# Optimization experiments

Hardware: AMD Instinct MI355X
Metric: run time of the kernel (lower is better)

The kernel has to match this reference:

```python
import jax, jax.numpy as jnp
import numpy as np

HEADS = 6
HEAD_DIM = 64
OUT_DIM = HEADS * HEAD_DIM  # 384
NEG_SLOPE = 0.2
VERY_NEG = -1e9  # fp32 path in original


def setup_inputs() -> dict:
    key = jax.random.key(0)
    k1, k2, k3, k4, k5 = jax.random.split(key, 5)
    N, IN_DIM = 2048, 256
    h = jax.random.normal(k1, (N, IN_DIM), dtype=jnp.float32)
    adj = jax.random.randint(k2, (N, N), 0, 2).astype(jnp.float32)
    adj = jnp.maximum(adj, jnp.eye(N, dtype=jnp.float32))  # self-loops
    W_src = jax.random.normal(k3, (HEADS, IN_DIM, HEAD_DIM), dtype=jnp.float32) * 0.05
    W_dst = jax.random.normal(k4, (HEADS, IN_DIM, HEAD_DIM), dtype=jnp.float32) * 0.05
    a = jax.random.normal(k5, (HEADS, HEAD_DIM), dtype=jnp.float32) * 0.05
    bias = jnp.zeros((OUT_DIM,), dtype=jnp.float32)
    return {"h": h, "adj": adj, "W_src": W_src, "W_dst": W_dst, "a": a, "bias": bias}


def _gatv2(h, adj, W_src, W_dst, a, bias):
    N = h.shape[0]
    mask = adj > 0  # (N, N)
    Q = jnp.einsum('nd,hdf->hnf', h, W_src)  # (H, N, F)
    K = jnp.einsum('nd,hdf->hnf', h, W_dst)  # (H, N, F)
    outs, attns = [], []
    for i in range(HEADS):  # loop over small fixed head count to cap (N,N,F) intermediates
        s = Q[i][:, None, :] + K[i][None, :, :]          # (N, N, F)
        s = jnp.where(s >= 0, s, NEG_SLOPE * s)          # LeakyReLU
        e = jnp.einsum('ijf,f->ij', s, a[i])             # (N, N)
        e = jnp.where(mask, e, VERY_NEG)
        p = jax.nn.softmax(e, axis=-1)                   # stable (max-subtract) as in original
        outs.append(p @ K[i])                            # (N, F)
        attns.append(p)
    out = jnp.stack(outs, axis=0)                        # (H, N, F)
    h_prime = out.transpose(1, 0, 2).reshape(N, OUT_DIM) + bias  # concat heads
    attn_mean = jnp.mean(jnp.stack(attns, axis=0), axis=0)       # (N, N)
    return h_prime, attn_mean


def reference(h, adj, W_src, W_dst, a, bias):
    return _gatv2(h, adj, W_src, W_dst, a, bias)
```

## Files before the change

kernel.cpp:

```cpp
#include <hip/hip_runtime.h>

namespace {

constexpr int N_NODES = 2048;
constexpr int IN_DIM  = 256;
constexpr int HEADS   = 6;
constexpr int HD      = 64;
constexpr int OUT_DIM = HEADS * HD;

__global__ __launch_bounds__(64) void qk_proj(
    const float* __restrict__ hmat, const float* __restrict__ Wsrc,
    const float* __restrict__ Wdst, const float* __restrict__ a,
    float* __restrict__ Qw, float* __restrict__ Kw,
    float* __restrict__ qaw, float* __restrict__ kaw)
{
  const int f    = threadIdx.x;
  const int i    = blockIdx.x;
  const int head = blockIdx.y;
  const int z    = blockIdx.z;
  const float* __restrict__ W = (z ? Wdst : Wsrc) + (size_t)head * IN_DIM * HD;
  const float* __restrict__ hrow = hmat + (size_t)i * IN_DIM;

  float a0 = 0.f, a1 = 0.f, a2 = 0.f, a3 = 0.f;
  #pragma unroll 4
  for (int k = 0; k < IN_DIM; k += 4) {
    a0 = fmaf(hrow[k + 0], W[(k + 0) * HD + f], a0);
    a1 = fmaf(hrow[k + 1], W[(k + 1) * HD + f], a1);
    a2 = fmaf(hrow[k + 2], W[(k + 2) * HD + f], a2);
    a3 = fmaf(hrow[k + 3], W[(k + 3) * HD + f], a3);
  }
  const float acc = (a0 + a1) + (a2 + a3);
  (z ? Kw : Qw)[((size_t)head * N_NODES + i) * HD + f] = acc;

  float rsum = acc * a[head * HD + f];
  #pragma unroll
  for (int off = 32; off; off >>= 1) rsum += __shfl_xor(rsum, off);
  if (f == 0) (z ? kaw : qaw)[head * N_NODES + i] = 0.6f * rsum;
}

__global__ __launch_bounds__(256, 1) void gat_fused(
    const float* __restrict__ Qw, const float* __restrict__ Kw,
    const float* __restrict__ qaw, const float* __restrict__ kaw,
    const float* __restrict__ a, const float* __restrict__ adj,
    const float* __restrict__ bias, float* __restrict__ out_h,
    float* __restrict__ out_attn)
{
  __shared__ float e_lds[8][N_NODES];
  __shared__ float Kt[128][65];
  __shared__ float Qs[8][64];
  __shared__ float a04[64];

  const int t  = threadIdx.x;
  const int r  = t >> 5;
  const int jj = t & 31;
  const int i0 = blockIdx.x * 8;

  for (int hh = 0; hh < HEADS; ++hh) {
    __syncthreads();
    for (int idx = t; idx < 512; idx += 256)
      Qs[idx >> 6][idx & 63] =
          Qw[((size_t)hh * N_NODES + i0 + (idx >> 6)) * HD + (idx & 63)];
    if (t < 64) a04[t] = 0.4f * a[hh * HD + t];
    __syncthreads();

    const float qa_r = qaw[hh * N_NODES + i0 + r];

    float m = -1e30f;
    for (int jt = 0; jt < 16; ++jt) {
      const int j0 = jt << 7;
      __syncthreads();
      #pragma unroll
      for (int q = 0; q < 8; ++q) {
        const int f4 = t + (q << 8);
        const int row = f4 >> 4, c = (f4 & 15) << 2;
        const float4 v = *(const float4*)&Kw[((size_t)hh * N_NODES + j0 + row) * HD + c];
        Kt[row][c] = v.x; Kt[row][c + 1] = v.y; Kt[row][c + 2] = v.z; Kt[row][c + 3] = v.w;
      }
      __syncthreads();
      #pragma unroll
      for (int k = 0; k < 4; ++k) {
        const int j  = jj + (k << 5);
        const int jg = j0 + j;
        float A = 0.f;
        #pragma unroll
        for (int f0 = 0; f0 < 64; f0 += 4) {
          const float4 av = *(const float4*)&a04[f0];
          const float4 qv = *(const float4*)&Qs[r][f0];
          A = fmaf(fabsf(qv.x + Kt[j][f0 + 0]), av.x, A);
          A = fmaf(fabsf(qv.y + Kt[j][f0 + 1]), av.y, A);
          A = fmaf(fabsf(qv.z + Kt[j][f0 + 2]), av.z, A);
          A = fmaf(fabsf(qv.w + Kt[j][f0 + 3]), av.w, A);
        }
        const float ad  = adj[(size_t)(i0 + r) * N_NODES + jg];
        const float kaj = kaw[hh * N_NODES + jg];
        const float e = (ad > 0.f) ? (A + qa_r + kaj) : -1e30f;
        e_lds[r][jg] = e;
        m = fmaxf(m, e);
      }
    }
    #pragma unroll
    for (int off = 16; off; off >>= 1) m = fmaxf(m, __shfl_xor(m, off));

    float s0 = 0.f, s1 = 0.f, s2 = 0.f, s3 = 0.f;
    for (int jt = 0; jt < 16; ++jt) {
      const int j0 = jt << 7;
      const float v0 = __expf(e_lds[r][j0 + jj +  0] - m);
      const float v1 = __expf(e_lds[r][j0 + jj + 32] - m);
      const float v2 = __expf(e_lds[r][j0 + jj + 64] - m);
      const float v3 = __expf(e_lds[r][j0 + jj + 96] - m);
      e_lds[r][j0 + jj +  0] = v0;
      e_lds[r][j0 + jj + 32] = v1;
      e_lds[r][j0 + jj + 64] = v2;
      e_lds[r][j0 + jj + 96] = v3;
      s0 += v0; s1 += v1; s2 += v2; s3 += v3;
    }
    float s = (s0 + s1) + (s2 + s3);
    #pragma unroll
    for (int off = 16; off; off >>= 1) s += __shfl_xor(s, off);
    const float inv_s = 1.0f / s;
    __syncthreads();

    const int f0 = jj << 1, f1 = f0 + 1;
    float pv0a = 0.f, pv0b = 0.f, pv1a = 0.f, pv1b = 0.f;
    for (int jt = 0; jt < 16; ++jt) {
      const int j0 = jt << 7;
      #pragma unroll
      for (int q = 0; q < 8; ++q) {
        const int f4 = t + (q << 8);
        const int row = f4 >> 4, c = (f4 & 15) << 2;
        const float4 v = *(const float4*)&Kw[((size_t)hh * N_NODES + j0 + row) * HD + c];
        Kt[row][c] = v.x; Kt[row][c + 1] = v.y; Kt[row][c + 2] = v.z; Kt[row][c + 3] = v.w;
      }
      #pragma unroll
      for (int k = 0; k < 4; ++k) {
        const int jg = j0 + jj + (k << 5);
        const float p = e_lds[r][jg] * inv_s;
        const size_t ai = (size_t)(i0 + r) * N_NODES + jg;
        if (hh == 0)               out_attn[ai] = p;
        else if (hh == HEADS - 1)  out_attn[ai] = (out_attn[ai] + p) * (1.0f / 6.0f);
        else                       out_attn[ai] += p;
      }
      __syncthreads();
      #pragma unroll 4
      for (int j2 = 0; j2 < 128; j2 += 2) {
        const float va = e_lds[r][j0 + j2];
        const float vb = e_lds[r][j0 + j2 + 1];
        pv0a = fmaf(va, Kt[j2][f0],     pv0a);
        pv1a = fmaf(va, Kt[j2][f1],     pv1a);
        pv0b = fmaf(vb, Kt[j2 + 1][f0], pv0b);
        pv1b = fmaf(vb, Kt[j2 + 1][f1], pv1b);
      }
      __syncthreads();
    }
    out_h[(size_t)(i0 + r) * OUT_DIM + hh * HD + f0] =
        (pv0a + pv0b) * inv_s + bias[hh * HD + f0];
    out_h[(size_t)(i0 + r) * OUT_DIM + hh * HD + f1] =
        (pv1a + pv1b) * inv_s + bias[hh * HD + f1];
  }
}

}

extern "C" void kernel_launch(void* const* d_in, const int* in_sizes, int n_in,
                              void* d_out, int out_size, void* d_ws, size_t ws_size,
                              hipStream_t stream) {
  const float* hmat = (const float*)d_in[0];
  const float* adj  = (const float*)d_in[1];
  const float* Wsrc = (const float*)d_in[2];
  const float* Wdst = (const float*)d_in[3];
  const float* a    = (const float*)d_in[4];
  const float* bias = (const float*)d_in[5];

  float* out_h    = (float*)d_out;
  float* out_attn = out_h + (size_t)N_NODES * OUT_DIM;

  float* Qw  = (float*)d_ws;
  float* Kw  = Qw + (size_t)HEADS * N_NODES * HD;
  float* qaw = Kw + (size_t)HEADS * N_NODES * HD;
  float* kaw = qaw + HEADS * N_NODES;

  qk_proj<<<dim3(N_NODES, HEADS, 2), 64, 0, stream>>>(hmat, Wsrc, Wdst, a,
                                                      Qw, Kw, qaw, kaw);
  gat_fused<<<dim3(N_NODES / 8), 256, 0, stream>>>(Qw, Kw, qaw, kaw, a, adj,
                                                   bias, out_h, out_attn);
}
```

Measured before the change: 862.0 us.

## Restructure GATv2 kernel: register-tiled scores, bitmask adjacency, direct global K reads

```diff
diff --git a/kernel.cpp b/kernel.cpp
--- a/kernel.cpp
+++ b/kernel.cpp
@@ -8,14 +8,15 @@
 constexpr int HD      = 64;
 constexpr int OUT_DIM = HEADS * HD;
 
-__global__ __launch_bounds__(64) void qk_proj(
+__global__ __launch_bounds__(256) void qk_proj(
     const float* __restrict__ hmat, const float* __restrict__ Wsrc,
     const float* __restrict__ Wdst, const float* __restrict__ a,
     float* __restrict__ Qw, float* __restrict__ Kw,
     float* __restrict__ qaw, float* __restrict__ kaw)
 {
-  const int f    = threadIdx.x;
-  const int i    = blockIdx.x;
+  const int lane = threadIdx.x & 63;
+  const int w    = threadIdx.x >> 6;
+  const int i    = blockIdx.x * 4 + w;
   const int head = blockIdx.y;
   const int z    = blockIdx.z;
   const float* __restrict__ W = (z ? Wdst : Wsrc) + (size_t)head * IN_DIM * HD;
@@ -24,21 +25,22 @@
   float a0 = 0.f, a1 = 0.f, a2 = 0.f, a3 = 0.f;
   #pragma unroll 4
   for (int k = 0; k < IN_DIM; k += 4) {
-    a0 = fmaf(hrow[k + 0], W[(k + 0) * HD + f], a0);
-    a1 = fmaf(hrow[k + 1], W[(k + 1) * HD + f], a1);
-    a2 = fmaf(hrow[k + 2], W[(k + 2) * HD + f], a2);
-    a3 = fmaf(hrow[k + 3], W[(k + 3) * HD + f], a3);
+    const float4 hv = *(const float4*)&hrow[k];
+    a0 = fmaf(hv.x, W[(k + 0) * HD + lane], a0);
+    a1 = fmaf(hv.y, W[(k + 1) * HD + lane], a1);
+    a2 = fmaf(hv.z, W[(k + 2) * HD + lane], a2);
+    a3 = fmaf(hv.w, W[(k + 3) * HD + lane], a3);
   }
   const float acc = (a0 + a1) + (a2 + a3);
-  (z ? Kw : Qw)[((size_t)head * N_NODES + i) * HD + f] = acc;
-
-  float rsum = acc * a[head * HD + f];
+  (z ? Kw : Qw)[((size_t)head * N_NODES + i) * HD + lane] = acc;
+
+  float rsum = acc * a[head * HD + lane];
   #pragma unroll
   for (int off = 32; off; off >>= 1) rsum += __shfl_xor(rsum, off);
-  if (f == 0) (z ? kaw : qaw)[head * N_NODES + i] = 0.6f * rsum;
-}
-
-__global__ __launch_bounds__(256, 1) void gat_fused(
+  if (lane == 0) (z ? kaw : qaw)[head * N_NODES + i] = 0.6f * rsum;
+}
+
+__global__ __launch_bounds__(512, 2) void gat_fused(
     const float* __restrict__ Qw, const float* __restrict__ Kw,
     const float* __restrict__ qaw, const float* __restrict__ kaw,
     const float* __restrict__ a, const float* __restrict__ adj,
@@ -46,116 +48,177 @@
     float* __restrict__ out_attn)
 {
   __shared__ float e_lds[8][N_NODES];
-  __shared__ float Kt[128][65];
   __shared__ float Qs[8][64];
   __shared__ float a04[64];
-
-  const int t  = threadIdx.x;
-  const int r  = t >> 5;
-  const int jj = t & 31;
-  const int i0 = blockIdx.x * 8;
+  __shared__ float qas[8];
+  __shared__ float msh[8], invs[8];
+  __shared__ float red[8][8];
+  __shared__ unsigned long long mask_lds[8][32];
+
+  const int t    = threadIdx.x;
+  const int lane = t & 63;
+  const int wv   = t >> 6;
+  const int i0   = blockIdx.x * 8;
+
+  for (int c = 0; c < 32; ++c) {
+    const float ad = adj[(size_t)(i0 + wv) * N_NODES + c * 64 + lane];
+    const unsigned long long b = __ballot(ad > 0.f);
+    if (lane == 0) mask_lds[wv][c] = b;
+  }
 
   for (int hh = 0; hh < HEADS; ++hh) {
     __syncthreads();
-    for (int idx = t; idx < 512; idx += 256)
-      Qs[idx >> 6][idx & 63] =
-          Qw[((size_t)hh * N_NODES + i0 + (idx >> 6)) * HD + (idx & 63)];
+    Qs[t >> 6][t & 63] = Qw[((size_t)hh * N_NODES + i0 + (t >> 6)) * HD + (t & 63)];
     if (t < 64) a04[t] = 0.4f * a[hh * HD + t];
-    __syncthreads();
-
-    const float qa_r = qaw[hh * N_NODES + i0 + r];
-
-    float m = -1e30f;
-    for (int jt = 0; jt < 16; ++jt) {
-      const int j0 = jt << 7;
-      __syncthreads();
-      #pragma unroll
-      for (int q = 0; q < 8; ++q) {
-        const int f4 = t + (q << 8);
-        const int row = f4 >> 4, c = (f4 & 15) << 2;
-        const float4 v = *(const float4*)&Kw[((size_t)hh * N_NODES + j0 + row) * HD + c];
-        Kt[row][c] = v.x; Kt[row][c + 1] = v.y; Kt[row][c + 2] = v.z; Kt[row][c + 3] = v.w;
-      }
-      __syncthreads();
-      #pragma unroll
-      for (int k = 0; k < 4; ++k) {
-        const int j  = jj + (k << 5);
-        const int jg = j0 + j;
-        float A = 0.f;
+    if (t < 8)  qas[t] = qaw[hh * N_NODES + i0 + t];
+    __syncthreads();
+
+    float m[8];
+    #pragma unroll
+    for (int r = 0; r < 8; ++r) m[r] = -3e38f;
+
+    for (int jp = 0; jp < 2; ++jp) {
+      const int j0 = 2 * t + jp * 1024;
+      const float* __restrict__ Kp = Kw + ((size_t)hh * N_NODES + j0) * HD;
+      float acc[8][2] = {};
+      #pragma unroll
+      for (int fcb = 0; fcb < 2; ++fcb) {
         #pragma unroll
-        for (int f0 = 0; f0 < 64; f0 += 4) {
-          const float4 av = *(const float4*)&a04[f0];
-          const float4 qv = *(const float4*)&Qs[r][f0];
-          A = fmaf(fabsf(qv.x + Kt[j][f0 + 0]), av.x, A);
-          A = fmaf(fabsf(qv.y + Kt[j][f0 + 1]), av.y, A);
-          A = fmaf(fabsf(qv.z + Kt[j][f0 + 2]), av.z, A);
-          A = fmaf(fabsf(qv.w + Kt[j][f0 + 3]), av.w, A);
+        for (int fc = 0; fc < 8; ++fc) {
+          const int f = fcb * 32 + fc * 4;
+          const float4 kva = *(const float4*)&Kp[f];
+          const float4 kvb = *(const float4*)&Kp[64 + f];
+          const float4 av  = *(const float4*)&a04[f];
+          #pragma unroll
+          for (int r = 0; r < 8; ++r) {
+            const float4 qv = *(const float4*)&Qs[r][f];
+            acc[r][0] = fmaf(fabsf(qv.x + kva.x), av.x, acc[r][0]);
+            acc[r][0] = fmaf(fabsf(qv.y + kva.y), av.y, acc[r][0]);
+            acc[r][0] = fmaf(fabsf(qv.z + kva.z), av.z, acc[r][0]);
+            acc[r][0] = fmaf(fabsf(qv.w + kva.w), av.w, acc[r][0]);
+            acc[r][1] = fmaf(fabsf(qv.x + kvb.x), av.x, acc[r][1]);
+            acc[r][1] = fmaf(fabsf(qv.y + kvb.y), av.y, acc[r][1]);
+            acc[r][1] = fmaf(fabsf(qv.z + kvb.z), av.z, acc[r][1]);
+            acc[r][1] = fmaf(fabsf(qv.w + kvb.w), av.w, acc[r][1]);
+          }
         }
-        const float ad  = adj[(size_t)(i0 + r) * N_NODES + jg];
-        const float kaj = kaw[hh * N_NODES + jg];
-        const float e = (ad > 0.f) ? (A + qa_r + kaj) : -1e30f;
-        e_lds[r][jg] = e;
-        m = fmaxf(m, e);
-      }
-    }
-    #pragma unroll
-    for (int off = 16; off; off >>= 1) m = fmaxf(m, __shfl_xor(m, off));
-
-    float s0 = 0.f, s1 = 0.f, s2 = 0.f, s3 = 0.f;
-    for (int jt = 0; jt < 16; ++jt) {
-      const int j0 = jt << 7;
-      const float v0 = __expf(e_lds[r][j0 + jj +  0] - m);
-      const float v1 = __expf(e_lds[r][j0 + jj + 32] - m);
-      const float v2 = __expf(e_lds[r][j0 + jj + 64] - m);
-      const float v3 = __expf(e_lds[r][j0 + jj + 96] - m);
-      e_lds[r][j0 + jj +  0] = v0;
-      e_lds[r][j0 + jj + 32] = v1;
-      e_lds[r][j0 + jj + 64] = v2;
-      e_lds[r][j0 + jj + 96] = v3;
-      s0 += v0; s1 += v1; s2 += v2; s3 += v3;
-    }
-    float s = (s0 + s1) + (s2 + s3);
-    #pragma unroll
-    for (int off = 16; off; off >>= 1) s += __shfl_xor(s, off);
-    const float inv_s = 1.0f / s;
-    __syncthreads();
-
-    const int f0 = jj << 1, f1 = f0 + 1;
-    float pv0a = 0.f, pv0b = 0.f, pv1a = 0.f, pv1b = 0.f;
-    for (int jt = 0; jt < 16; ++jt) {
-      const int j0 = jt << 7;
-      #pragma unroll
-      for (int q = 0; q < 8; ++q) {
-        const int f4 = t + (q << 8);
-        const int row = f4 >> 4, c = (f4 & 15) << 2;
-        const float4 v = *(const float4*)&Kw[((size_t)hh * N_NODES + j0 + row) * HD + c];
-        Kt[row][c] = v.x; Kt[row][c + 1] = v.y; Kt[row][c + 2] = v.z; Kt[row][c + 3] = v.w;
-      }
-      #pragma unroll
-      for (int k = 0; k < 4; ++k) {
-        const int jg = j0 + jj + (k << 5);
-        const float p = e_lds[r][jg] * inv_s;
-        const size_t ai = (size_t)(i0 + r) * N_NODES + jg;
-        if (hh == 0)               out_attn[ai] = p;
-        else if (hh == HEADS - 1)  out_attn[ai] = (out_attn[ai] + p) * (1.0f / 6.0f);
-        else                       out_attn[ai] += p;
-      }
-      __syncthreads();
-      #pragma unroll 4
-      for (int j2 = 0; j2 < 128; j2 += 2) {
-        const float va = e_lds[r][j0 + j2];
-        const float vb = e_lds[r][j0 + j2 + 1];
-        pv0a = fmaf(va, Kt[j2][f0],     pv0a);
-        pv1a = fmaf(va, Kt[j2][f1],     pv1a);
-        pv0b = fmaf(vb, Kt[j2 + 1][f0], pv0b);
-        pv1b = fmaf(vb, Kt[j2 + 1][f1], pv1b);
-      }
-      __syncthreads();
-    }
-    out_h[(size_t)(i0 + r) * OUT_DIM + hh * HD + f0] =
-        (pv0a + pv0b) * inv_s + bias[hh * HD + f0];
-    out_h[(size_t)(i0 + r) * OUT_DIM + hh * HD + f1] =
-        (pv1a + pv1b) * inv_s + bias[hh * HD + f1];
+      }
+      const float2 kaj = *(const float2*)&kaw[hh * N_NODES + j0];
+      const int c = j0 >> 6;
+      const int b0 = j0 & 63, b1 = b0 + 1;
+      #pragma unroll
+      for (int r = 0; r < 8; ++r) {
+        const unsigned long long mw = mask_lds[r][c];
+        const float e0 = ((mw >> b0) & 1ull) ? acc[r][0] + qas[r] + kaj.x : -1e30f;
+        const float e1 = ((mw >> b1) & 1ull) ? acc[r][1] + qas[r] + kaj.y : -1e30f;
+        *(float2*)&e_lds[r][j0] = make_float2(e0, e1);
+        m[r] = fmaxf(m[r], fmaxf(e0, e1));
+      }
+    }
+    #pragma unroll
+    for (int r = 0; r < 8; ++r) {
+      float v = m[r];
+      #pragma unroll
+      for (int off = 32; off; off >>= 1) v = fmaxf(v, __shfl_xor(v, off));
+      if (lane == 0) red[r][wv] = v;
+    }
+    __syncthreads();
+    if (t < 8) {
+      float v = red[t][0];
+      #pragma unroll
+      for (int q = 1; q < 8; ++q) v = fmaxf(v, red[t][q]);
+      msh[t] = v;
+    }
+    __syncthreads();
+
+    float s[8];
+    #pragma unroll
+    for (int r = 0; r < 8; ++r) s[r] = 0.f;
+    #pragma unroll
+    for (int jp = 0; jp < 2; ++jp) {
+      const int j0 = 2 * t + jp * 1024;
+      #pragma unroll
+      for (int r = 0; r < 8; ++r) {
+        const float2 v = *(const float2*)&e_lds[r][j0];
+        const float mr = msh[r];
+        const float p0 = __expf(v.x - mr);
+        const float p1 = __expf(v.y - mr);
+        *(float2*)&e_lds[r][j0] = make_float2(p0, p1);
+        s[r] += p0 + p1;
+      }
+    }
+    #pragma unroll
+    for (int r = 0; r < 8; ++r) {
+      float v = s[r];
+      #pragma unroll
+      for (int off = 32; off; off >>= 1) v += __shfl_xor(v, off);
+      if (lane == 0) red[r][wv] = v;
+    }
+    __syncthreads();
+    if (t < 8) {
+      float v = red[t][0];
+      #pragma unroll
+      for (int q = 1; q < 8; ++q) v += red[t][q];
+      invs[t] = 1.0f / v;
+    }
+    __syncthreads();
+
+    #pragma unroll
+    for (int jp = 0; jp < 2; ++jp) {
+      const int j0 = 2 * t + jp * 1024;
+      #pragma unroll
+      for (int r = 0; r < 8; ++r) {
+        const float2 v = *(const float2*)&e_lds[r][j0];
+        const float iv = invs[r];
+        float2 p = make_float2(v.x * iv, v.y * iv);
+        float2* ap = (float2*)&out_attn[(size_t)(i0 + r) * N_NODES + j0];
+        if (hh == 0) {
+          *ap = p;
+        } else if (hh == HEADS - 1) {
+          const float2 po = *ap;
+          *ap = make_float2((po.x + p.x) * (1.0f / 6.0f),
+                            (po.y + p.y) * (1.0f / 6.0f));
+        } else {
+          const float2 po = *ap;
+          *ap = make_float2(po.x + p.x, po.y + p.y);
+        }
+      }
+    }
+
+    {
+      const int r  = wv;
+      const int fq = t & 15;
+      const int js = (t >> 4) & 3;
+      const float* __restrict__ Kp =
+          Kw + ((size_t)hh * N_NODES + js * 512) * HD + fq * 4;
+      const float* __restrict__ pp = &e_lds[r][js * 512];
+      float4 acc = make_float4(0.f, 0.f, 0.f, 0.f);
+      for (int j = 0; j < 512; j += 8) {
+        #pragma unroll
+        for (int u = 0; u < 8; ++u) {
+          const float p = pp[j + u];
+          const float4 kv = *(const float4*)&Kp[(size_t)(j + u) * HD];
+          acc.x = fmaf(p, kv.x, acc.x);
+          acc.y = fmaf(p, kv.y, acc.y);
+          acc.z = fmaf(p, kv.z, acc.z);
+          acc.w = fmaf(p, kv.w, acc.w);
+        }
+      }
+      acc.x += __shfl_xor(acc.x, 16); acc.x += __shfl_xor(acc.x, 32);
+      acc.y += __shfl_xor(acc.y, 16); acc.y += __shfl_xor(acc.y, 32);
+      acc.z += __shfl_xor(acc.z, 16); acc.z += __shfl_xor(acc.z, 32);
+      acc.w += __shfl_xor(acc.w, 16); acc.w += __shfl_xor(acc.w, 32);
+      if ((t & 63) < 16) {
+        const float iv = invs[r];
+        const float4 bv = *(const float4*)&bias[hh * 64 + fq * 4];
+        float4 o;
+        o.x = acc.x * iv + bv.x;
+        o.y = acc.y * iv + bv.y;
+        o.z = acc.z * iv + bv.z;
+        o.w = acc.w * iv + bv.w;
+        *(float4*)&out_h[(size_t)(i0 + r) * OUT_DIM + hh * 64 + fq * 4] = o;
+      }
+    }
   }
 }
 
@@ -179,8 +242,8 @@
   float* qaw = Kw + (size_t)HEADS * N_NODES * HD;
   float* kaw = qaw + HEADS * N_NODES;
 
-  qk_proj<<<dim3(N_NODES, HEADS, 2), 64, 0, stream>>>(hmat, Wsrc, Wdst, a,
-                                                      Qw, Kw, qaw, kaw);
-  gat_fused<<<dim3(N_NODES / 8), 256, 0, stream>>>(Qw, Kw, qaw, kaw, a, adj,
+  qk_proj<<<dim3(N_NODES / 4, HEADS, 2), 256, 0, stream>>>(hmat, Wsrc, Wdst, a,
+                                                           Qw, Kw, qaw, kaw);
+  gat_fused<<<dim3(N_NODES / 8), 512, 0, stream>>>(Qw, Kw, qaw, kaw, a, adj,
                                                    bias, out_h, out_attn);
 }
```

Result: slower. 2.212 ms (+156.6%).
